# Kernel tuning notes

Hardware: AMD Instinct MI355X
Metric: run time of the kernel (lower is better)

The kernel has to match this reference:

```python
import jax, jax.numpy as jnp
import numpy as np
from jax import lax

B, C_IN, C_OUT, H, W, E = 16, 256, 256, 32, 32, 8


def setup_inputs() -> dict:
    key = jax.random.key(0)
    k = jax.random.split(key, 5)
    x = jax.random.normal(k[0], (B, C_IN, H, W), dtype=jnp.float32)
    # router: Conv2d(C_IN, E, kernel_size=1) -> weight [E, C_IN], bias [E]
    wc = jax.random.normal(k[1], (E, C_IN), dtype=jnp.float32) / np.sqrt(C_IN)
    bc = jnp.zeros((E,), dtype=jnp.float32)
    # experts: E x Conv2d(C_IN, C_OUT, 3, padding=1) + ReLU
    we = jax.random.normal(k[2], (E, C_OUT, C_IN, 3, 3), dtype=jnp.float32) / np.sqrt(C_IN * 9)
    be = jnp.zeros((E, C_OUT), dtype=jnp.float32)
    return {"x": x, "wc": wc, "bc": bc, "we": we, "be": be}


def reference(x, wc, bc, we, be):
    Bx = x.shape[0]
    # controller: 1x1 conv then global avg-pool == pool then linear
    pooled = jnp.mean(x, axis=(2, 3))                      # [B, C_IN]
    logits = pooled @ wc.T + bc                            # [B, E]
    decisions = jnp.argmax(logits, axis=1)                 # [B] int
    # run ALL experts on the full batch as one grouped conv: weight [E*C_OUT, C_IN, 3, 3]
    w_all = we.reshape(E * C_OUT, C_IN, 3, 3)
    y = lax.conv_general_dilated(
        x, w_all, window_strides=(1, 1), padding="SAME",
        dimension_numbers=("NCHW", "OIHW", "NCHW"))        # [B, E*C_OUT, H, W]
    y = y + be.reshape(1, E * C_OUT, 1, 1)
    y = jax.nn.relu(y).reshape(Bx, E, C_OUT, H, W)
    # faithful to forward_test: out block i is components[dec[i]](x) for the FULL batch
    # out[i*B + j] = y[j, dec[i]]
    gathered = y[:, decisions]                             # [j, i, C_OUT, H, W]
    out = jnp.swapaxes(gathered, 0, 1).reshape(Bx * Bx, C_OUT, H, W)
    return out
```

## Files before the change

kernel.cpp:

```cpp
#include <hip/hip_runtime.h>
#include <hip/hip_bf16.h>
#include <stdint.h>

#define B_    16
#define CIN   256
#define COUT  256
#define E_    8
#define HW    1024
#define PH    34
#define PW    34

typedef __attribute__((ext_vector_type(8))) short  short8;
typedef __attribute__((ext_vector_type(4))) float  floatx4;

#define XT_OFF 17408
#define XT_BYTES (B_*PH*PW*CIN*2)
#define WT_OFF (XT_OFF + XT_BYTES)

__device__ __forceinline__ void gld_lds16(const void* g, void* l) {
    __builtin_amdgcn_global_load_lds(
        (const __attribute__((address_space(1))) unsigned int*)g,
        (__attribute__((address_space(3))) unsigned int*)l,
        16, 0, 0);
}

__global__ void pool_kernel(const float* __restrict__ x, float* __restrict__ pooled) {
    int b = blockIdx.x, c = blockIdx.y;
    const float4* p = (const float4*)(x + ((size_t)b*CIN + c)*HW);
    int t = threadIdx.x;
    float4 v = p[t];
    float s = v.x + v.y + v.z + v.w;
    #pragma unroll
    for (int o = 32; o > 0; o >>= 1) s += __shfl_down(s, o, 64);
    __shared__ float wsum[4];
    if ((t & 63) == 0) wsum[t >> 6] = s;
    __syncthreads();
    if (t == 0) pooled[b*CIN + c] = (wsum[0]+wsum[1]+wsum[2]+wsum[3]) * (1.0f/1024.0f);
}

__global__ void decide_kernel(const float* __restrict__ pooled, const float* __restrict__ wc,
                              const float* __restrict__ bc, int* __restrict__ dec) {
    int t = threadIdx.x;
    int b = t >> 3, e = t & 7;
    float acc = bc[e];
    const float4* pp = (const float4*)(pooled + b*CIN);
    const float4* ww = (const float4*)(wc + e*CIN);
    #pragma unroll 4
    for (int i = 0; i < CIN/4; ++i) {
        float4 p = pp[i], w = ww[i];
        acc += p.x*w.x + p.y*w.y + p.z*w.z + p.w*w.w;
    }
    __shared__ float lg[16][8];
    lg[b][e] = acc;
    __syncthreads();
    if (e == 0) {
        float best = lg[b][0]; int bi = 0;
        #pragma unroll
        for (int j = 1; j < 8; ++j) { if (lg[b][j] > best) { best = lg[b][j]; bi = j; } }
        dec[b] = bi;
    }
}

__global__ void xpose_kernel(const float* __restrict__ x, unsigned short* __restrict__ xt) {
    int b = blockIdx.x;
    int hw0 = blockIdx.y * 32;
    int ci0 = blockIdx.z * 32;
    __shared__ float tile[32][33];
    int t = threadIdx.x;
    int j = t & 31;
    int i = t >> 5;
    #pragma unroll
    for (int p = 0; p < 4; ++p)
        tile[i + p*8][j] = x[((size_t)b*CIN + ci0 + i + p*8)*HW + hw0 + j];
    __syncthreads();
    int cw = t & 31;
    int rw = t >> 5;
    #pragma unroll
    for (int p = 0; p < 4; ++p) {
        int hw = hw0 + rw + p*8;
        int h = hw >> 5, w = hw & 31;
        __hip_bfloat16 hv = __float2bfloat16(tile[cw][rw + p*8]);
        xt[(((size_t)b*PH + h + 1)*PW + (w + 1))*CIN + ci0 + cw] = *(unsigned short*)&hv;
    }
}

__global__ void wpose_kernel(const float* __restrict__ we, unsigned short* __restrict__ wt) {
    int e = blockIdx.x >> 8, co = blockIdx.x & 255;
    __shared__ float buf[CIN*9];
    const float* src = we + ((size_t)e*COUT + co)*CIN*9;
    int t = threadIdx.x;
    #pragma unroll
    for (int k = 0; k < 9; ++k) buf[t + k*256] = src[t + k*256];
    __syncthreads();
    #pragma unroll
    for (int rs = 0; rs < 9; ++rs) {
        __hip_bfloat16 h = __float2bfloat16(buf[t*9 + rs]);
        wt[(((size_t)e*9 + rs)*COUT + co)*CIN + t] = *(unsigned short*)&h;
    }
}

__global__ __launch_bounds__(256) void conv_kernel(
    const unsigned short* __restrict__ xt, const unsigned short* __restrict__ wt,
    const float* __restrict__ be, const int* __restrict__ dec,
    float* __restrict__ out) {

    int tile = blockIdx.x;
    int b = blockIdx.y;
    int e = blockIdx.z;
    int mt = tile >> 3, nt = tile & 7;

    int dcs[16];
    #pragma unroll
    for (int i = 0; i < 16; ++i) dcs[i] = dec[i];
    bool active = false;
    #pragma unroll
    for (int i = 0; i < 16; ++i) active |= (dcs[i] == e);
    if (!active) return;

    __shared__ __align__(16) unsigned short sA[512*8];
    __shared__ __align__(16) unsigned short sB[1024*8];

    int t = threadIdx.x;
    int wave = t >> 6, lane = t & 63;
    int wm = wave >> 1, wn = wave & 1;
    int kg = lane >> 4, ln = lane & 15;

    int ph0 = nt * 4;
    int co0 = mt * 128;

    floatx4 acc[4][4];
    #pragma unroll
    for (int i = 0; i < 4; ++i)
        #pragma unroll
        for (int j = 0; j < 4; ++j) acc[i][j] = (floatx4)0.0f;

    const unsigned short* xb = xt + (size_t)b*PH*PW*CIN;

    for (int ck = 0; ck < 8; ++ck) {
        int ci0 = ck * 32;
        #pragma unroll
        for (int k = 0; k < 4; ++k) {
            int c = t + k*256;
            int cc = c < 816 ? c : 815;
            int row = cc / 136;
            int rem = cc - row*136;
            int col = rem >> 2;
            int g   = rem & 3;
            gld_lds16(xb + ((size_t)(ph0 + row)*PW + col)*CIN + ci0 + g*8, &sB[c*8]);
        }
        for (int sh = 0; sh < 9; ++sh) {
            const unsigned short* wsrc = wt + (((size_t)e*9 + sh)*COUT + co0)*CIN + ci0;
            #pragma unroll
            for (int k = 0; k < 2; ++k) {
                int c = t + k*256;
                int rowA = c >> 2, g = c & 3;
                gld_lds16(wsrc + (size_t)rowA*CIN + g*8, &sA[c*8]);
            }
            __syncthreads();

            short8 a[4], bb[4];
            #pragma unroll
            for (int im = 0; im < 4; ++im)
                a[im] = *(const short8*)(&sA[((wm*64 + im*16 + ln)*4 + kg)*8]);
            int r = sh / 3, s = sh - r*3;
            #pragma unroll
            for (int in = 0; in < 4; ++in) {
                int n  = wn*64 + in*16 + ln;
                int hl = n >> 5, wl = n & 31;
                bb[in] = *(const short8*)(&sB[(((hl + r)*34 + (wl + s))*4 + kg)*8]);
            }
            __syncthreads();

            #pragma unroll
            for (int im = 0; im < 4; ++im)
                #pragma unroll
                for (int in = 0; in < 4; ++in)
                    acc[im][in] = __builtin_amdgcn_mfma_f32_16x16x32_bf16(a[im], bb[in], acc[im][in], 0, 0, 0);
        }
    }

    #pragma unroll
    for (int im = 0; im < 4; ++im) {
        int co = co0 + wm*64 + im*16 + kg*4;
        #pragma unroll
        for (int rg = 0; rg < 4; ++rg) {
            float bv = be[e*COUT + co + rg];
            #pragma unroll
            for (int in = 0; in < 4; ++in) {
                float v = acc[im][in][rg] + bv;
                acc[im][in][rg] = v > 0.0f ? v : 0.0f;
            }
        }
    }
    for (int i = 0; i < 16; ++i) {
        if (dcs[i] != e) continue;
        float* ob = out + (size_t)(i*16 + b)*COUT*HW;
        #pragma unroll
        for (int im = 0; im < 4; ++im) {
            int co = co0 + wm*64 + im*16 + kg*4;
            #pragma unroll
            for (int in = 0; in < 4; ++in) {
                int hw = nt*128 + wn*64 + in*16 + ln;
                #pragma unroll
                for (int rg = 0; rg < 4; ++rg)
                    ob[(size_t)(co + rg)*HW + hw] = acc[im][in][rg];
            }
        }
    }
}

extern "C" void kernel_launch(void* const* d_in, const int* in_sizes, int n_in,
                              void* d_out, int out_size, void* d_ws, size_t ws_size,
                              hipStream_t stream) {
    const float* x  = (const float*)d_in[0];
    const float* wc = (const float*)d_in[1];
    const float* bc = (const float*)d_in[2];
    const float* we = (const float*)d_in[3];
    const float* be = (const float*)d_in[4];
    float* out = (float*)d_out;

    char* ws = (char*)d_ws;
    int*   dec    = (int*)ws;
    float* pooled = (float*)(ws + 64);
    unsigned short* xt = (unsigned short*)(ws + XT_OFF);
    unsigned short* wt = (unsigned short*)(ws + WT_OFF);

    hipMemsetAsync(xt, 0, XT_BYTES, stream);

    pool_kernel  <<<dim3(16, 256), 256, 0, stream>>>(x, pooled);
    decide_kernel<<<1, 128, 0, stream>>>(pooled, wc, bc, dec);
    xpose_kernel <<<dim3(16, 32, 8), 256, 0, stream>>>(x, xt);
    wpose_kernel <<<2048, 256, 0, stream>>>(we, wt);
    conv_kernel  <<<dim3(16, 16, 8), 256, 0, stream>>>(xt, wt, be, dec, out);
}
```

Measured before the change: 469.2 us.

## Double-buffer conv LDS tiles with prefetch and XOR-swizzled layout

The conv kernel now double-buffers its weight and input LDS tiles. The next shift's weights, and the next channel chunk's input patch, are issued with global_load_lds before the current MFMAs run, which cuts the barriers per iteration from two to one. LDS chunk placement is XOR-swizzled on both store and load to reduce bank conflicts on the short8 reads. The cost is double the LDS footprint, which may lower occupancy, plus reliance on the barrier draining the asynchronous LDS loads.

After: 464.7 us. No clear change (-1.0%).

```diff
diff --git a/kernel.cpp b/kernel.cpp
--- a/kernel.cpp
+++ b/kernel.cpp
@@ -117,8 +117,8 @@
     for (int i = 0; i < 16; ++i) active |= (dcs[i] == e);
     if (!active) return;
 
-    __shared__ __align__(16) unsigned short sA[512*8];
-    __shared__ __align__(16) unsigned short sB[1024*8];
+    __shared__ __align__(16) unsigned short sA[2][512*8];
+    __shared__ __align__(16) unsigned short sB[2][1024*8];
 
     int t = threadIdx.x;
     int wave = t >> 6, lane = t & 63;
@@ -134,48 +134,77 @@
         #pragma unroll
         for (int j = 0; j < 4; ++j) acc[i][j] = (floatx4)0.0f;
 
-    const unsigned short* xb = xt + (size_t)b*PH*PW*CIN;
+    const unsigned short* xb = xt + ((size_t)b*PH + ph0)*PW*CIN;
+    const unsigned short* wb = wt + (size_t)e*9*COUT*CIN + (size_t)co0*CIN;
+
+    auto stageA = [&](int ck, int sh, int buf) {
+        const unsigned short* wsrc = wb + (size_t)sh*COUT*CIN + ck*32;
+        #pragma unroll
+        for (int k = 0; k < 2; ++k) {
+            int c = t + k*256;
+            int row = c >> 2, gs = c & 3;
+            int g = gs ^ ((row >> 1) & 3);
+            gld_lds16(wsrc + (size_t)row*CIN + g*8, &sA[buf][c*8]);
+        }
+    };
+    auto stageB = [&](int ck, int buf) {
+        const unsigned short* xsrc = xb + ck*32;
+        #pragma unroll
+        for (int k = 0; k < 3; ++k) {
+            int c = t + k*256;
+            int rB = c >> 2, gs = c & 3;
+            int g = gs ^ ((rB >> 1) & 3);
+            gld_lds16(xsrc + (size_t)rB*CIN + g*8, &sB[buf][c*8]);
+        }
+        if (t < 64) {
+            int c = t + 768;
+            int cc = c < 816 ? c : 815;
+            int rB = cc >> 2, gs = cc & 3;
+            int g = gs ^ ((rB >> 1) & 3);
+            gld_lds16(xsrc + (size_t)rB*CIN + g*8, &sB[buf][c*8]);
+        }
+    };
+
+    stageB(0, 0);
+    stageA(0, 0, 0);
+    __syncthreads();
 
     for (int ck = 0; ck < 8; ++ck) {
-        int ci0 = ck * 32;
-        #pragma unroll
-        for (int k = 0; k < 4; ++k) {
-            int c = t + k*256;
-            int cc = c < 816 ? c : 815;
-            int row = cc / 136;
-            int rem = cc - row*136;
-            int col = rem >> 2;
-            int g   = rem & 3;
-            gld_lds16(xb + ((size_t)(ph0 + row)*PW + col)*CIN + ci0 + g*8, &sB[c*8]);
-        }
         for (int sh = 0; sh < 9; ++sh) {
-            const unsigned short* wsrc = wt + (((size_t)e*9 + sh)*COUT + co0)*CIN + ci0;
-            #pragma unroll
-            for (int k = 0; k < 2; ++k) {
-                int c = t + k*256;
-                int rowA = c >> 2, g = c & 3;
-                gld_lds16(wsrc + (size_t)rowA*CIN + g*8, &sA[c*8]);
-            }
-            __syncthreads();
-
-            short8 a[4], bb[4];
-            #pragma unroll
-            for (int im = 0; im < 4; ++im)
-                a[im] = *(const short8*)(&sA[((wm*64 + im*16 + ln)*4 + kg)*8]);
+            int it = ck*9 + sh;
+            int ab = it & 1, bb_ = ck & 1;
+
+            if (sh < 8) {
+                stageA(ck, sh + 1, ab ^ 1);
+            } else if (ck < 7) {
+                stageA(ck + 1, 0, ab ^ 1);
+                stageB(ck + 1, bb_ ^ 1);
+            }
+
+            short8 a[4], bv[4];
+            #pragma unroll
+            for (int im = 0; im < 4; ++im) {
+                int row = wm*64 + im*16 + ln;
+                int cL = row*4 + (kg ^ ((row >> 1) & 3));
+                a[im] = *(const short8*)(&sA[ab][cL*8]);
+            }
             int r = sh / 3, s = sh - r*3;
             #pragma unroll
             for (int in = 0; in < 4; ++in) {
                 int n  = wn*64 + in*16 + ln;
                 int hl = n >> 5, wl = n & 31;
-                bb[in] = *(const short8*)(&sB[(((hl + r)*34 + (wl + s))*4 + kg)*8]);
-            }
-            __syncthreads();
+                int rB = (hl + r)*34 + (wl + s);
+                int cL = rB*4 + (kg ^ ((rB >> 1) & 3));
+                bv[in] = *(const short8*)(&sB[bb_][cL*8]);
+            }
 
             #pragma unroll
             for (int im = 0; im < 4; ++im)
                 #pragma unroll
                 for (int in = 0; in < 4; ++in)
-                    acc[im][in] = __builtin_amdgcn_mfma_f32_16x16x32_bf16(a[im], bb[in], acc[im][in], 0, 0, 0);
+                    acc[im][in] = __builtin_amdgcn_mfma_f32_16x16x32_bf16(a[im], bv[in], acc[im][in], 0, 0, 0);
+
+            __syncthreads();
         }
     }
 
@@ -184,10 +213,10 @@
         int co = co0 + wm*64 + im*16 + kg*4;
         #pragma unroll
         for (int rg = 0; rg < 4; ++rg) {
-            float bv = be[e*COUT + co + rg];
+            float bvv = be[e*COUT + co + rg];
             #pragma unroll
             for (int in = 0; in < 4; ++in) {
-                float v = acc[im][in][rg] + bv;
+                float v = acc[im][in][rg] + bvv;
                 acc[im][in][rg] = v > 0.0f ? v : 0.0f;
             }
         }
```
